# Performance work log

Hardware: AMD Instinct MI355X
Metric: run time of the kernel (lower is better)

Reference implementation:

```python
import jax, jax.numpy as jnp
import numpy as np
import math

B, S, E, H = 2, 2048, 1024, 16
D = E // H
# neuromodulator levels (deterministic branch choices)
NA, ACH, DA = 0.5, 0.5, -0.5

def setup_inputs() -> dict:
    key = jax.random.key(0)
    ks = jax.random.split(key, 12)
    xav = lambda k, i, o: jax.random.uniform(k, (i, o), jnp.float32, -1.0, 1.0) * math.sqrt(6.0 / (i + o))
    return {
        'query': jax.random.normal(ks[0], (B, S, E), jnp.float32),
        'key':   jax.random.normal(ks[1], (B, S, E), jnp.float32),
        'value': jax.random.normal(ks[2], (B, S, E), jnp.float32),
        'Wq': xav(ks[3], E, E), 'bq': jnp.zeros((E,), jnp.float32),
        'Wk': xav(ks[4], E, E), 'bk': jnp.zeros((E,), jnp.float32),
        'Wv': xav(ks[5], E, E), 'bv': jnp.zeros((E,), jnp.float32),
        'Wo': xav(ks[6], E, E), 'bo': jnp.zeros((E,), jnp.float32),
        'time_scales': jnp.ones((H,), jnp.float32),
    }

def reference(query, key, value, Wq, bq, Wk, bk, Wv, bv, Wo, bo, time_scales):
    # projections -> [B, H, S, D]
    q = (query @ Wq + bq).reshape(B, S, H, D).transpose(0, 2, 1, 3)
    k = (key   @ Wk + bk).reshape(B, S, H, D).transpose(0, 2, 1, 3)
    v = (value @ Wv + bv).reshape(B, S, H, D).transpose(0, 2, 1, 3)
    # per-head time-scale on keys
    k = k * time_scales[None, :, None, None]
    scores = jnp.einsum('bhtd,bhsd->bhts', q, k) / math.sqrt(D)
    # noradrenaline: temperature scaling
    temperature = 1.0 / (1.0 + NA * 0.5)
    scores = scores / temperature
    # acetylcholine: boost diagonal
    diag = jnp.eye(S, dtype=scores.dtype)[None, None]
    scores = scores * (1.0 + ACH * 0.3 * diag)
    kk = max(1, int(S * 0.2))
    topv = jax.lax.top_k(scores, kk)[0]          # [B,H,S,kk]
    min_topk = topv[..., -1:]                     # kth largest
    mask = (scores >= min_topk).astype(scores.dtype)
    scores = scores * (1.0 + (-DA) * 0.3 * mask)
    attn = jax.nn.softmax(scores, axis=-1)
    out = jnp.einsum('bhts,bhsd->bhtd', attn, v)
    out = out.transpose(0, 2, 1, 3).reshape(B, S, E)
    out = out @ Wo + bo
    return out
```

## Files before the change

### kernel.cpp

```cpp
#include <hip/hip_runtime.h>
#include <cstdint>
#include <cstddef>

#define BB 2
#define SS 2048
#define EE 1024
#define HH 16
#define DH 64
#define KKSEL 409
#define QT 16
#define PST 136

typedef __attribute__((ext_vector_type(8))) short bf16x8;
typedef __attribute__((ext_vector_type(4))) float f32x4;
typedef unsigned short ushort_t;

__device__ __forceinline__ unsigned short f2bf(float f){
    unsigned u = __float_as_uint(f);
    u += 0x7fffu + ((u >> 16) & 1u);
    return (unsigned short)(u >> 16);
}
__device__ __forceinline__ float bf2f(unsigned short h){
    return __uint_as_float(((unsigned)h) << 16);
}
__device__ __forceinline__ unsigned sortkey(float f){
    unsigned u = __float_as_uint(f);
    return (u & 0x80000000u) ? ~u : (u | 0x80000000u);
}
__device__ __forceinline__ float inv_sortkey(unsigned k){
    unsigned u = (k & 0x80000000u) ? (k & 0x7fffffffu) : ~k;
    return __uint_as_float(u);
}
__device__ __forceinline__ void split8(const float* f, bf16x8& h, bf16x8& l){
    #pragma unroll
    for (int j = 0; j < 8; ++j){
        ushort_t hh = f2bf(f[j]);
        h[j] = (short)hh;
        l[j] = (short)f2bf(f[j] - bf2f(hh));
    }
}

__device__ __forceinline__ float topk_thresh(const float* cand){
    float mx = cand[0], mn = cand[0];
    #pragma unroll
    for (int j = 1; j < 32; ++j){
        mx = fmaxf(mx, cand[j]);
        mn = fminf(mn, cand[j]);
    }
    #pragma unroll
    for (int off = 1; off < 64; off <<= 1){
        mx = fmaxf(mx, __shfl_xor(mx, off, 64));
        mn = fminf(mn, __shfl_xor(mn, off, 64));
    }
    unsigned lo = sortkey(mn), hi = sortkey(mx) + 1u;
    #pragma unroll 1
    for (int it = 0; it < 20 && (hi - lo) > 1u; ++it){
        const unsigned span = hi - lo;
        const unsigned p1 = lo + (span >> 2);
        const unsigned p2 = lo + (span >> 1);
        const unsigned p3 = p2 + (span >> 2);
        const float f1 = inv_sortkey(p1);
        const float f2 = inv_sortkey(p2);
        const float f3 = inv_sortkey(p3);
        int c1 = 0, c2 = 0, c3 = 0;
        #pragma unroll
        for (int j = 0; j < 32; ++j){
            c1 += (int)__popcll(__ballot(cand[j] >= f1));
            c2 += (int)__popcll(__ballot(cand[j] >= f2));
            c3 += (int)__popcll(__ballot(cand[j] >= f3));
        }
        if (c1 == KKSEL){ lo = p1; break; }
        if (c2 == KKSEL){ lo = p2; break; }
        if (c3 == KKSEL){ lo = p3; break; }
        if (c1 < KKSEL)       hi = p1;
        else if (c2 < KKSEL){ lo = p1; hi = p2; }
        else if (c3 < KKSEL){ lo = p2; hi = p3; }
        else                  lo = p3;
    }
    return inv_sortkey(lo);
}

struct CvtArgs {
    const float* W[4];
    ushort_t* H[4];
    ushort_t* L[4];
};

__global__ __launch_bounds__(256) void convert_wt4(CvtArgs a)
{
    __shared__ float T[64][65];
    const int z = blockIdx.z;
    const float* __restrict__ W = a.W[z];
    ushort_t* __restrict__ Ht = a.H[z];
    ushort_t* __restrict__ Lt = a.L[z];

    const int tid = threadIdx.x;
    const int ty = tid >> 4, tx = tid & 15;
    const int n0 = blockIdx.x * 64, k0 = blockIdx.y * 64;
    #pragma unroll
    for (int i = 0; i < 4; ++i){
        const int kl = ty + i * 16;
        float4 w = *(const float4*)&W[(size_t)(k0 + kl) * EE + n0 + tx * 4];
        T[kl][tx*4 + 0] = w.x; T[kl][tx*4 + 1] = w.y;
        T[kl][tx*4 + 2] = w.z; T[kl][tx*4 + 3] = w.w;
    }
    __syncthreads();
    #pragma unroll
    for (int i = 0; i < 4; ++i){
        const int nl = ty + i * 16;
        ushort4 h, l;
        ushort_t* hp = &h.x; ushort_t* lp = &l.x;
        #pragma unroll
        for (int j = 0; j < 4; ++j){
            const float v = T[tx*4 + j][nl];
            ushort_t hh = f2bf(v);
            hp[j] = hh;
            lp[j] = f2bf(v - bf2f(hh));
        }
        const size_t o = (size_t)(n0 + nl) * EE + k0 + tx * 4;
        *(ushort4*)&Ht[o] = h;
        *(ushort4*)&Lt[o] = l;
    }
}

template<int MODE>
__device__ __forceinline__ void gemm_body(
        const float* __restrict__ X,
        const ushort_t* __restrict__ Wth, const ushort_t* __restrict__ Wtl,
        const float* __restrict__ bias, const float* __restrict__ ts,
        float* __restrict__ OutF, ushort_t* __restrict__ OutH,
        ushort_t* __restrict__ OutL, ushort_t* buf)
{
    const int tid  = threadIdx.x;
    const int lane = tid & 63, wave = tid >> 6;
    const int c16  = lane & 15, qd = lane >> 4;
    const int m0 = blockIdx.y * 128, n0 = blockIdx.x * 128;
    const int wm = (wave >> 1) * 64, wn = (wave & 1) * 64;
    const int lrow = tid >> 1, lkg = (tid & 1) * 16;

    f32x4 acc[4][4];
    #pragma unroll
    for (int a = 0; a < 4; ++a)
        #pragma unroll
        for (int b = 0; b < 4; ++b) acc[a][b] = (f32x4){0.f,0.f,0.f,0.f};

    const float* Xr = X + (size_t)(m0 + lrow) * EE + lkg;
    const ushort_t* Whr = Wth + (size_t)(n0 + lrow) * EE + lkg;
    const ushort_t* Wlr = Wtl + (size_t)(n0 + lrow) * EE + lkg;

    {
        float fx[16];
        *(float4*)&fx[0]  = *(const float4*)&Xr[0];
        *(float4*)&fx[4]  = *(const float4*)&Xr[4];
        *(float4*)&fx[8]  = *(const float4*)&Xr[8];
        *(float4*)&fx[12] = *(const float4*)&Xr[12];
        bf16x8 w0 = *(const bf16x8*)&Whr[0];
        bf16x8 w1 = *(const bf16x8*)&Whr[8];
        bf16x8 w2 = *(const bf16x8*)&Wlr[0];
        bf16x8 w3 = *(const bf16x8*)&Wlr[8];
        bf16x8 h0, l0, h1, l1;
        split8(fx, h0, l0); split8(fx + 8, h1, l1);
        ushort_t* S = buf;
        *(bf16x8*)&S[lrow*32 + lkg]           = h0;
        *(bf16x8*)&S[lrow*32 + lkg + 8]       = h1;
        *(bf16x8*)&S[4096 + lrow*32 + lkg]    = l0;
        *(bf16x8*)&S[4096 + lrow*32 + lkg+8]  = l1;
        *(bf16x8*)&S[8192 + lrow*32 + lkg]    = w0;
        *(bf16x8*)&S[8192 + lrow*32 + lkg+8]  = w1;
        *(bf16x8*)&S[12288 + lrow*32 + lkg]   = w2;
        *(bf16x8*)&S[12288 + lrow*32 + lkg+8] = w3;
    }
    __syncthreads();

    int cur = 0;
    for (int k0 = 0; k0 < EE; k0 += 32){
        const bool more = (k0 + 32) < EE;
        float fx[16];
        bf16x8 gw[4];
        if (more){
            const float* xp = Xr + k0 + 32;
            *(float4*)&fx[0]  = *(const float4*)&xp[0];
            *(float4*)&fx[4]  = *(const float4*)&xp[4];
            *(float4*)&fx[8]  = *(const float4*)&xp[8];
            *(float4*)&fx[12] = *(const float4*)&xp[12];
            gw[0] = *(const bf16x8*)&Whr[k0 + 32];
            gw[1] = *(const bf16x8*)&Whr[k0 + 40];
            gw[2] = *(const bf16x8*)&Wlr[k0 + 32];
            gw[3] = *(const bf16x8*)&Wlr[k0 + 40];
        }
        const ushort_t* S  = buf + cur * 16384;
        const ushort_t* A0 = S;
        const ushort_t* A1 = S + 4096;
        const ushort_t* B0 = S + 8192;
        const ushort_t* B1 = S + 12288;
        bf16x8 afh[4], afl[4], bfh[4], bfl[4];
        #pragma unroll
        for (int i = 0; i < 4; ++i){
            afh[i] = *(const bf16x8*)&A0[(wm + i*16 + c16)*32 + qd*8];
            afl[i] = *(const bf16x8*)&A1[(wm + i*16 + c16)*32 + qd*8];
            bfh[i] = *(const bf16x8*)&B0[(wn + i*16 + c16)*32 + qd*8];
            bfl[i] = *(const bf16x8*)&B1[(wn + i*16 + c16)*32 + qd*8];
        }
        __builtin_amdgcn_s_setprio(1);
        #pragma unroll
        for (int a = 0; a < 4; ++a){
            #pragma unroll
            for (int b = 0; b < 4; ++b){
                if (MODE == 2){
                    acc[a][b] = __builtin_amdgcn_mfma_f32_16x16x32_bf16(afh[a], bfh[b], acc[a][b], 0,0,0);
                    acc[a][b] = __builtin_amdgcn_mfma_f32_16x16x32_bf16(afh[a], bfl[b], acc[a][b], 0,0,0);
                    acc[a][b] = __builtin_amdgcn_mfma_f32_16x16x32_bf16(afl[a], bfh[b], acc[a][b], 0,0,0);
                } else {
                    acc[a][b] = __builtin_amdgcn_mfma_f32_16x16x32_bf16(bfh[a], afh[b], acc[a][b], 0,0,0);
                    acc[a][b] = __builtin_amdgcn_mfma_f32_16x16x32_bf16(bfh[a], afl[b], acc[a][b], 0,0,0);
                    acc[a][b] = __builtin_amdgcn_mfma_f32_16x16x32_bf16(bfl[a], afh[b], acc[a][b], 0,0,0);
                }
            }
        }
        __builtin_amdgcn_s_setprio(0);
        if (more){
            bf16x8 h0, l0, h1, l1;
            split8(fx, h0, l0); split8(fx + 8, h1, l1);
            ushort_t* N = buf + (cur ^ 1) * 16384;
            *(bf16x8*)&N[lrow*32 + lkg]           = h0;
            *(bf16x8*)&N[lrow*32 + lkg + 8]       = h1;
            *(bf16x8*)&N[4096 + lrow*32 + lkg]    = l0;
            *(bf16x8*)&N[4096 + lrow*32 + lkg+8]  = l1;
            *(bf16x8*)&N[8192 + lrow*32 + lkg]    = gw[0];
            *(bf16x8*)&N[8192 + lrow*32 + lkg+8]  = gw[1];
            *(bf16x8*)&N[12288 + lrow*32 + lkg]   = gw[2];
            *(bf16x8*)&N[12288 + lrow*32 + lkg+8] = gw[3];
            __syncthreads();
            cur ^= 1;
        }
    }

    if (MODE == 3){
        #pragma unroll
        for (int a = 0; a < 4; ++a){
            const int ng = n0 + wn + a*16 + qd*4;
            float4 b4 = *(const float4*)&bias[ng];
            const float bb[4] = {b4.x, b4.y, b4.z, b4.w};
            #pragma unroll
            for (int b = 0; b < 4; ++b){
                const int mg = m0 + wm + b*16 + c16;
                float4 o;
                o.x = acc[a][b][0] + bb[0]; o.y = acc[a][b][1] + bb[1];
                o.z = acc[a][b][2] + bb[2]; o.w = acc[a][b][3] + bb[3];
                *(float4*)&OutF[(size_t)mg * EE + ng] = o;
            }
        }
    } else if (MODE == 0){
        #pragma unroll
        for (int a = 0; a < 4; ++a){
            const int ng = n0 + wn + a*16 + qd*4;
            const int h = ng >> 6, d0 = ng & 63;
            float4 b4 = *(const float4*)&bias[ng];
            const float bb[4] = {b4.x, b4.y, b4.z, b4.w};
            #pragma unroll
            for (int b = 0; b < 4; ++b){
                const int mg = m0 + wm + b*16 + c16;
                const int bi = mg >> 11, s = mg & (SS - 1);
                ushort4 hv, lv;
                ushort_t* hp = &hv.x; ushort_t* lp = &lv.x;
                #pragma unroll
                for (int r = 0; r < 4; ++r){
                    const float v = (acc[a][b][r] + bb[r]) * 0.15625f;
                    ushort_t hh = f2bf(v);
                    hp[r] = hh;
                    lp[r] = f2bf(v - bf2f(hh));
                }
                const size_t o = (((size_t)(bi * HH + h)) * SS + s) * DH + d0;
                *(ushort4*)&OutH[o] = hv;
                *(ushort4*)&OutL[o] = lv;
            }
        }
    } else if (MODE == 1){
        #pragma unroll
        for (int a = 0; a < 4; ++a){
            const int ng = n0 + wn + a*16 + qd*4;
            const int h = ng >> 6, d0 = ng & 63;
            const float tsc = ts[h];
            float4 b4 = *(const float4*)&bias[ng];
            const float bb[4] = {b4.x, b4.y, b4.z, b4.w};
            #pragma unroll
            for (int b = 0; b < 4; ++b){
                const int mg = m0 + wm + b*16 + c16;
                const int bi = mg >> 11, s = mg & (SS - 1);
                ushort4 hv;
                ushort_t* hp = &hv.x;
                #pragma unroll
                for (int r = 0; r < 4; ++r)
                    hp[r] = f2bf((acc[a][b][r] + bb[r]) * tsc);
                *(ushort4*)&OutH[(((size_t)(bi * HH + h)) * SS + s) * DH + d0] = hv;
            }
        }
    } else {
        #pragma unroll
        for (int a = 0; a < 4; ++a){
            const int mg = m0 + wm + a*16 + qd*4;
            const int bi = mg >> 11, s0 = mg & (SS - 1);
            #pragma unroll
            for (int b = 0; b < 4; ++b){
                const int ng = n0 + wn + b*16 + c16;
                const int h = ng >> 6, d = ng & 63;
                const float bv = bias[ng];
                ushort4 hv;
                ushort_t* hp = &hv.x;
                #pragma unroll
                for (int r = 0; r < 4; ++r) hp[r] = f2bf(acc[a][b][r] + bv);
                *(ushort4*)&OutH[(((size_t)(bi * HH + h)) * DH + d) * SS + s0] = hv;
            }
        }
    }
}

__global__ __launch_bounds__(256) void gemm_qkv(
        const float* __restrict__ q, const float* __restrict__ k,
        const float* __restrict__ v,
        const ushort_t* __restrict__ Wqh, const ushort_t* __restrict__ Wql,
        const ushort_t* __restrict__ Wkh, const ushort_t* __restrict__ Wkl,
        const ushort_t* __restrict__ Wvh, const ushort_t* __restrict__ Wvl,
        const float* __restrict__ bq, const float* __restrict__ bk,
        const float* __restrict__ bv, const float* __restrict__ ts,
        ushort_t* __restrict__ Qh, ushort_t* __restrict__ Ql,
        ushort_t* __restrict__ Kh, ushort_t* __restrict__ Vth)
{
    __shared__ ushort_t buf[2 * 16384];
    const int z = blockIdx.z;
    if (z == 0)
        gemm_body<0>(q, Wqh, Wql, bq, nullptr, nullptr, Qh, Ql, buf);
    else if (z == 1)
        gemm_body<1>(k, Wkh, Wkl, bk, ts, nullptr, Kh, nullptr, buf);
    else
        gemm_body<2>(v, Wvh, Wvl, bv, nullptr, nullptr, Vth, nullptr, buf);
}

__global__ __launch_bounds__(256) void gemm_out(
        const float* __restrict__ X,
        const ushort_t* __restrict__ Wth, const ushort_t* __restrict__ Wtl,
        const float* __restrict__ bias, float* __restrict__ OutF)
{
    __shared__ ushort_t buf[2 * 16384];
    gemm_body<3>(X, Wth, Wtl, bias, nullptr, OutF, nullptr, nullptr, buf);
}

__global__ __launch_bounds__(512, 4) void attn_kernel(
        const ushort_t* __restrict__ Qh, const ushort_t* __restrict__ Ql,
        const ushort_t* __restrict__ Khi, const ushort_t* __restrict__ Vth,
        float* __restrict__ AO)
{
    __shared__ __align__(16) char uni[65536];
    __shared__ float wsums[8][16];
    __shared__ float thr16[16];

    const int tid  = threadIdx.x;
    const int lane = tid & 63;
    const int wave = tid >> 6;
    const int qd   = lane >> 4;
    const int c16  = lane & 15;
    const unsigned Bx = blockIdx.x;
    const int xcd  = Bx & 7;
    const int qq   = Bx >> 3;
    const int tile = qq & 127;
    const int bh   = (qq >> 7) * 8 + xcd;
    const int t0   = tile * QT;
    const int wbase = wave * 256;

    bf16x8 qh[2], ql[2];
    {
        const size_t qbase = ((size_t)bh * SS + t0 + c16) * DH;
        #pragma unroll
        for (int kc = 0; kc < 2; ++kc){
            qh[kc] = *(const bf16x8*)&Qh[qbase + kc*32 + qd*8];
            ql[kc] = *(const bf16x8*)&Ql[qbase + kc*32 + qd*8];
        }
    }

    f32x4 acc[16];
    const ushort_t* Kh = Khi + (size_t)bh * SS * DH;
    __builtin_amdgcn_s_setprio(1);
    #pragma unroll
    for (int t = 0; t < 16; ++t){
        f32x4 a = {0.f, 0.f, 0.f, 0.f};
        const int srow = wbase + t*16 + c16;
        const ushort_t* kp = Kh + (size_t)srow * DH + qd*8;
        #pragma unroll
        for (int kc = 0; kc < 2; ++kc){
            bf16x8 kh = *(const bf16x8*)(kp + kc*32);
            a = __builtin_amdgcn_mfma_f32_16x16x32_bf16(qh[kc], kh, a, 0, 0, 0);
            a = __builtin_amdgcn_mfma_f32_16x16x32_bf16(ql[kc], kh, a, 0, 0, 0);
        }
        acc[t] = a;
    }
    __builtin_amdgcn_s_setprio(0);

    if (wave == (t0 >> 8)){
        #pragma unroll
        for (int t = 0; t < 16; ++t){
            const int colg = wbase + t*16 + c16;
            #pragma unroll
            for (int r = 0; r < 4; ++r)
                if (colg == t0 + qd*4 + r) acc[t][r] *= 1.15f;
        }
    }

    float* ex = (float*)uni;
    if (qd < 2){
        const int rl = (qd & 1) * 4;
        #pragma unroll
        for (int t = 0; t < 16; ++t)
            #pragma unroll
            for (int r = 0; r < 4; ++r)
                ex[(rl + r) * SS + wbase + t*16 + c16] = acc[t][r];
    }
    __syncthreads();
    float cand[32];
    #pragma unroll
    for (int j = 0; j < 32; ++j)
        cand[j] = ex[wave * SS + lane + 64*j];
    __syncthreads();
    if (qd >= 2){
        const int rl = (qd & 1) * 4;
        #pragma unroll
        for (int t = 0; t < 16; ++t)
            #pragma unroll
            for (int r = 0; r < 4; ++r)
                ex[(rl + r) * SS + wbase + t*16 + c16] = acc[t][r];
    }
    {
        const float th0 = topk_thresh(cand);
        if (lane == 0) thr16[wave] = th0;
    }
    __syncthreads();
    #pragma unroll
    for (int j = 0; j < 32; ++j)
        cand[j] = ex[wave * SS + lane + 64*j];
    {
        const float th1 = topk_thresh(cand);
        if (lane == 0) thr16[8 + wave] = th1;
    }
    __syncthreads();

    float thr[4];
    #pragma unroll
    for (int r = 0; r < 4; ++r) thr[r] = thr16[qd*4 + r];
    float psum[4] = {0.f, 0.f, 0.f, 0.f};
    #pragma unroll
    for (int t = 0; t < 16; ++t){
        #pragma unroll
        for (int r = 0; r < 4; ++r){
            float s = acc[t][r];
            s *= (s >= thr[r]) ? 1.15f : 1.0f;
            const float e = __expf(s);
            acc[t][r] = e;
            psum[r] += e;
        }
    }
    #pragma unroll
    for (int off = 1; off <= 8; off <<= 1){
        #pragma unroll
        for (int r = 0; r < 4; ++r) psum[r] += __shfl_xor(psum[r], off, 64);
    }
    if (c16 == 0){
        #pragma unroll
        for (int r = 0; r < 4; ++r) wsums[wave][qd*4 + r] = psum[r];
    }
    __syncthreads();
    float pinv[4];
    #pragma unroll
    for (int r = 0; r < 4; ++r){
        const int row = qd*4 + r;
        float s = 0.f;
        #pragma unroll
        for (int w = 0; w < 8; ++w) s += wsums[w][row];
        pinv[r] = 1.f / s;
    }

    const ushort_t* Vh = Vth + (size_t)bh * DH * SS;
    ushort_t* pw = (ushort_t*)uni + wave * (QT * PST);
    f32x4 oacc[4];
    #pragma unroll
    for (int dt = 0; dt < 4; ++dt) oacc[dt] = (f32x4){0.f, 0.f, 0.f, 0.f};

    #pragma unroll
    for (int half = 0; half < 2; ++half){
        #pragma unroll
        for (int tt = 0; tt < 8; ++tt){
            const int t = half*8 + tt;
            #pragma unroll
            for (int r = 0; r < 4; ++r)
                pw[(qd*4 + r) * PST + tt*16 + c16] = f2bf(acc[t][r] * pinv[r]);
        }
        #pragma unroll
        for (int kc = 0; kc < 4; ++kc){
            bf16x8 pf = *(const bf16x8*)&pw[c16 * PST + kc*32 + qd*8];
            const int sbase = wbase + half*128 + kc*32 + qd*8;
            __builtin_amdgcn_s_setprio(1);
            #pragma unroll
            for (int dt = 0; dt < 4; ++dt){
                const int d = dt*16 + c16;
                bf16x8 vh = *(const bf16x8*)(Vh + (size_t)d * SS + sbase);
                oacc[dt] = __builtin_amdgcn_mfma_f32_16x16x32_bf16(pf, vh, oacc[dt], 0, 0, 0);
            }
            __builtin_amdgcn_s_setprio(0);
        }
    }

    __syncthreads();
    float* red = (float*)uni;
    #pragma unroll
    for (int dt = 0; dt < 4; ++dt)
        #pragma unroll
        for (int r = 0; r < 4; ++r)
            red[(wave*16 + qd*4 + r) * 65 + dt*16 + c16] = oacc[dt][r];
    __syncthreads();

    const int b = bh >> 4, h = bh & 15;
    {
        const int r  = tid >> 5;
        const int c2 = (tid & 31) * 2;
        float s0 = 0.f, s1 = 0.f;
        #pragma unroll
        for (int w = 0; w < 8; ++w){
            s0 += red[(w*16 + r) * 65 + c2];
            s1 += red[(w*16 + r) * 65 + c2 + 1];
        }
        float2 o; o.x = s0; o.y = s1;
        *(float2*)&AO[((size_t)b * SS + t0 + r) * EE + h*DH + c2] = o;
    }
}

extern "C" void kernel_launch(void* const* d_in, const int* in_sizes, int n_in,
                              void* d_out, int out_size, void* d_ws, size_t ws_size,
                              hipStream_t stream)
{
    const float* query = (const float*)d_in[0];
    const float* key   = (const float*)d_in[1];
    const float* value = (const float*)d_in[2];
    const float* Wq    = (const float*)d_in[3];
    const float* bq    = (const float*)d_in[4];
    const float* Wk    = (const float*)d_in[5];
    const float* bk    = (const float*)d_in[6];
    const float* Wv    = (const float*)d_in[7];
    const float* bv    = (const float*)d_in[8];
    const float* Wo    = (const float*)d_in[9];
    const float* bo    = (const float*)d_in[10];
    const float* ts    = (const float*)d_in[11];
    float* out = (float*)d_out;
    char* w = (char*)d_ws;

    const size_t MB = 1u << 20;
    ushort_t* Qh  = (ushort_t*)(w + 0 * MB);
    ushort_t* Ql  = (ushort_t*)(w + 8 * MB);
    ushort_t* Kh  = (ushort_t*)(w + 16 * MB);
    ushort_t* Vth = (ushort_t*)(w + 24 * MB);
    float*    AOw = (float*)   (w + 32 * MB);
    ushort_t* Wqh = (ushort_t*)(w + 32 * MB);
    ushort_t* Wql = (ushort_t*)(w + 34 * MB);
    ushort_t* Wkh = (ushort_t*)(w + 36 * MB);
    ushort_t* Wkl = (ushort_t*)(w + 38 * MB);
    ushort_t* Wvh = (ushort_t*)(w + 40 * MB);
    ushort_t* Wvl = (ushort_t*)(w + 42 * MB);
    ushort_t* Woh = (ushort_t*)(w + 48 * MB);
    ushort_t* Wol = (ushort_t*)(w + 50 * MB);

    CvtArgs ca;
    ca.W[0] = Wq;  ca.W[1] = Wk;  ca.W[2] = Wv;  ca.W[3] = Wo;
    ca.H[0] = Wqh; ca.H[1] = Wkh; ca.H[2] = Wvh; ca.H[3] = Woh;
    ca.L[0] = Wql; ca.L[1] = Wkl; ca.L[2] = Wvl; ca.L[3] = Wol;

    hipLaunchKernelGGL(convert_wt4, dim3(16, 16, 4), dim3(256), 0, stream, ca);
    hipLaunchKernelGGL(gemm_qkv, dim3(8, 32, 3), dim3(256), 0, stream,
                       query, key, value, Wqh, Wql, Wkh, Wkl, Wvh, Wvl,
                       bq, bk, bv, ts, Qh, Ql, Kh, Vth);
    hipLaunchKernelGGL(attn_kernel, dim3(BB * HH * (SS / QT)), dim3(512), 0, stream,
                       Qh, Ql, Kh, Vth, AOw);
    hipLaunchKernelGGL(gemm_out, dim3(8, 32), dim3(256), 0, stream,
                       AOw, Woh, Wol, bo, out);
}
```

Before: 712.2 us.

## Load weight tiles directly to LDS, simplify top-k bisection, drop setprio hints

The GEMM's bf16 weight hi/lo tiles are now copied straight from global memory into LDS with global_load_lds, replacing the register round trip, while the fp32 activations are still split in registers. The top-k threshold search changes from a three-pivot quartering search to a plain binary bisection, which needs fewer ballot counts per step but more steps. All s_setprio hints around the MFMA loops are removed, and the exp mask multiply is rewritten slightly. Direct LDS loads free registers and issue slots, but their ordering against the existing barrier and any pending global loads is an added correctness concern.

```diff
diff --git a/kernel.cpp b/kernel.cpp
--- a/kernel.cpp
+++ b/kernel.cpp
@@ -39,6 +39,11 @@
         l[j] = (short)f2bf(f[j] - bf2f(hh));
     }
 }
+__device__ __forceinline__ void gload_lds16(const ushort_t* g, ushort_t* l){
+    __builtin_amdgcn_global_load_lds(
+        (const __attribute__((address_space(1))) void*)g,
+        (__attribute__((address_space(3))) void*)l, 16, 0, 0);
+}
 
 __device__ __forceinline__ float topk_thresh(const float* cand){
     float mx = cand[0], mn = cand[0];
@@ -54,28 +59,15 @@
     }
     unsigned lo = sortkey(mn), hi = sortkey(mx) + 1u;
     #pragma unroll 1
-    for (int it = 0; it < 20 && (hi - lo) > 1u; ++it){
-        const unsigned span = hi - lo;
-        const unsigned p1 = lo + (span >> 2);
-        const unsigned p2 = lo + (span >> 1);
-        const unsigned p3 = p2 + (span >> 2);
-        const float f1 = inv_sortkey(p1);
-        const float f2 = inv_sortkey(p2);
-        const float f3 = inv_sortkey(p3);
-        int c1 = 0, c2 = 0, c3 = 0;
-        #pragma unroll
-        for (int j = 0; j < 32; ++j){
-            c1 += (int)__popcll(__ballot(cand[j] >= f1));
-            c2 += (int)__popcll(__ballot(cand[j] >= f2));
-            c3 += (int)__popcll(__ballot(cand[j] >= f3));
-        }
-        if (c1 == KKSEL){ lo = p1; break; }
-        if (c2 == KKSEL){ lo = p2; break; }
-        if (c3 == KKSEL){ lo = p3; break; }
-        if (c1 < KKSEL)       hi = p1;
-        else if (c2 < KKSEL){ lo = p1; hi = p2; }
-        else if (c3 < KKSEL){ lo = p2; hi = p3; }
-        else                  lo = p3;
+    for (int it = 0; it < 32 && (hi - lo) > 1u; ++it){
+        const unsigned mid = lo + ((hi - lo) >> 1);
+        const float midf = inv_sortkey(mid);
+        int c = 0;
+        #pragma unroll
+        for (int j = 0; j < 32; ++j)
+            c += (int)__popcll(__ballot(cand[j] >= midf));
+        if (c == KKSEL){ lo = mid; break; }
+        if (c > KKSEL) lo = mid; else hi = mid;
     }
     return inv_sortkey(lo);
 }
@@ -145,30 +137,32 @@
         for (int b = 0; b < 4; ++b) acc[a][b] = (f32x4){0.f,0.f,0.f,0.f};
 
     const float* Xr = X + (size_t)(m0 + lrow) * EE + lkg;
-    const ushort_t* Whr = Wth + (size_t)(n0 + lrow) * EE + lkg;
-    const ushort_t* Wlr = Wtl + (size_t)(n0 + lrow) * EE + lkg;
+
+    const int seg0 = wave * 2, seg1 = wave * 2 + 1;
+    const size_t wofs0 = (size_t)(n0 + seg0*16 + (lane >> 2)) * EE + (lane & 3) * 8;
+    const size_t wofs1 = (size_t)(n0 + seg1*16 + (lane >> 2)) * EE + (lane & 3) * 8;
+    const ushort_t* WhA = Wth + wofs0;
+    const ushort_t* WhB = Wth + wofs1;
+    const ushort_t* WlA = Wtl + wofs0;
+    const ushort_t* WlB = Wtl + wofs1;
 
     {
+        ushort_t* S = buf;
+        gload_lds16(WhA, S + 8192  + seg0*512);
+        gload_lds16(WhB, S + 8192  + seg1*512);
+        gload_lds16(WlA, S + 12288 + seg0*512);
+        gload_lds16(WlB, S + 12288 + seg1*512);
         float fx[16];
         *(float4*)&fx[0]  = *(const float4*)&Xr[0];
         *(float4*)&fx[4]  = *(const float4*)&Xr[4];
         *(float4*)&fx[8]  = *(const float4*)&Xr[8];
         *(float4*)&fx[12] = *(const float4*)&Xr[12];
-        bf16x8 w0 = *(const bf16x8*)&Whr[0];
-        bf16x8 w1 = *(const bf16x8*)&Whr[8];
-        bf16x8 w2 = *(const bf16x8*)&Wlr[0];
-        bf16x8 w3 = *(const bf16x8*)&Wlr[8];
         bf16x8 h0, l0, h1, l1;
         split8(fx, h0, l0); split8(fx + 8, h1, l1);
-        ushort_t* S = buf;
         *(bf16x8*)&S[lrow*32 + lkg]           = h0;
         *(bf16x8*)&S[lrow*32 + lkg + 8]       = h1;
         *(bf16x8*)&S[4096 + lrow*32 + lkg]    = l0;
         *(bf16x8*)&S[4096 + lrow*32 + lkg+8]  = l1;
-        *(bf16x8*)&S[8192 + lrow*32 + lkg]    = w0;
-        *(bf16x8*)&S[8192 + lrow*32 + lkg+8]  = w1;
-        *(bf16x8*)&S[12288 + lrow*32 + lkg]   = w2;
-        *(bf16x8*)&S[12288 + lrow*32 + lkg+8] = w3;
     }
     __syncthreads();
 
@@ -176,17 +170,18 @@
     for (int k0 = 0; k0 < EE; k0 += 32){
         const bool more = (k0 + 32) < EE;
         float fx[16];
-        bf16x8 gw[4];
         if (more){
-            const float* xp = Xr + k0 + 32;
+            const int kt = k0 + 32;
+            ushort_t* N = buf + (cur ^ 1) * 16384;
+            gload_lds16(WhA + kt, N + 8192  + seg0*512);
+            gload_lds16(WhB + kt, N + 8192  + seg1*512);
+            gload_lds16(WlA + kt, N + 12288 + seg0*512);
+            gload_lds16(WlB + kt, N + 12288 + seg1*512);
+            const float* xp = Xr + kt;
             *(float4*)&fx[0]  = *(const float4*)&xp[0];
             *(float4*)&fx[4]  = *(const float4*)&xp[4];
             *(float4*)&fx[8]  = *(const float4*)&xp[8];
             *(float4*)&fx[12] = *(const float4*)&xp[12];
-            gw[0] = *(const bf16x8*)&Whr[k0 + 32];
-            gw[1] = *(const bf16x8*)&Whr[k0 + 40];
-            gw[2] = *(const bf16x8*)&Wlr[k0 + 32];
-            gw[3] = *(const bf16x8*)&Wlr[k0 + 40];
         }
         const ushort_t* S  = buf + cur * 16384;
         const ushort_t* A0 = S;
@@ -201,7 +196,6 @@
             bfh[i] = *(const bf16x8*)&B0[(wn + i*16 + c16)*32 + qd*8];
             bfl[i] = *(const bf16x8*)&B1[(wn + i*16 + c16)*32 + qd*8];
         }
-        __builtin_amdgcn_s_setprio(1);
         #pragma unroll
         for (int a = 0; a < 4; ++a){
             #pragma unroll
@@ -217,7 +211,6 @@
                 }
             }
         }
-        __builtin_amdgcn_s_setprio(0);
         if (more){
             bf16x8 h0, l0, h1, l1;
             split8(fx, h0, l0); split8(fx + 8, h1, l1);
@@ -226,10 +219,6 @@
             *(bf16x8*)&N[lrow*32 + lkg + 8]       = h1;
             *(bf16x8*)&N[4096 + lrow*32 + lkg]    = l0;
             *(bf16x8*)&N[4096 + lrow*32 + lkg+8]  = l1;
-            *(bf16x8*)&N[8192 + lrow*32 + lkg]    = gw[0];
-            *(bf16x8*)&N[8192 + lrow*32 + lkg+8]  = gw[1];
-            *(bf16x8*)&N[12288 + lrow*32 + lkg]   = gw[2];
-            *(bf16x8*)&N[12288 + lrow*32 + lkg+8] = gw[3];
             __syncthreads();
             cur ^= 1;
         }
@@ -379,7 +368,6 @@
 
     f32x4 acc[16];
     const ushort_t* Kh = Khi + (size_t)bh * SS * DH;
-    __builtin_amdgcn_s_setprio(1);
     #pragma unroll
     for (int t = 0; t < 16; ++t){
         f32x4 a = {0.f, 0.f, 0.f, 0.f};
@@ -393,7 +381,6 @@
         }
         acc[t] = a;
     }
-    __builtin_amdgcn_s_setprio(0);
 
     if (wave == (t0 >> 8)){
         #pragma unroll
@@ -450,9 +437,9 @@
     for (int t = 0; t < 16; ++t){
         #pragma unroll
         for (int r = 0; r < 4; ++r){
-            float s = acc[t][r];
-            s *= (s >= thr[r]) ? 1.15f : 1.0f;
-            const float e = __expf(s);
+            const float s = acc[t][r];
+            const float m = (s >= thr[r]) ? 1.15f : 1.0f;
+            const float e = __expf(s * m);
             acc[t][r] = e;
             psum[r] += e;
         }
@@ -496,14 +483,12 @@
         for (int kc = 0; kc < 4; ++kc){
             bf16x8 pf = *(const bf16x8*)&pw[c16 * PST + kc*32 + qd*8];
             const int sbase = wbase + half*128 + kc*32 + qd*8;
-            __builtin_amdgcn_s_setprio(1);
             #pragma unroll
             for (int dt = 0; dt < 4; ++dt){
                 const int d = dt*16 + c16;
                 bf16x8 vh = *(const bf16x8*)(Vh + (size_t)d * SS + sbase);
                 oacc[dt] = __builtin_amdgcn_mfma_f32_16x16x32_bf16(pf, vh, oacc[dt], 0, 0, 0);
             }
-            __builtin_amdgcn_s_setprio(0);
         }
     }
 
```

Measured after the change: 671.5 us. 1.06x faster.
